# Performance work log

Measured on AMD Instinct MI355X. Metric: run time of the kernel, lower is better.

Reference implementation:

```python
import jax, jax.numpy as jnp
import numpy as np

B, L, H = 2, 2048, 1024
NH, HD = 16, 64  # n_heads, head_size


def setup_inputs() -> dict:
    key = jax.random.key(0)
    ks = jax.random.split(key, 12)
    scale = 1.0 / np.sqrt(H)
    inp = {
        "hidden_states": jax.random.normal(ks[0], (B, L, H), dtype=jnp.float32),
        "tau": jax.random.uniform(ks[1], (B, 1), dtype=jnp.float32) + 0.5,
        "delta": jax.random.normal(ks[2], (B, L), dtype=jnp.float32) * 0.1,
        "Wq": jax.random.normal(ks[3], (H, H), dtype=jnp.float32) * scale,
        "bq": jnp.zeros((H,), dtype=jnp.float32),
        "Wk": jax.random.normal(ks[4], (H, H), dtype=jnp.float32) * scale,
        "bk": jnp.zeros((H,), dtype=jnp.float32),
        "Wv": jax.random.normal(ks[5], (H, H), dtype=jnp.float32) * scale,
        "bv": jnp.zeros((H,), dtype=jnp.float32),
        "Wo": jax.random.normal(ks[6], (H, H), dtype=jnp.float32) * scale,
        "bo": jnp.zeros((H,), dtype=jnp.float32),
    }
    return inp


def _split_heads(x):
    # [B, L, H] -> [B, NH, L, HD]
    return x.reshape(B, L, NH, HD).transpose(0, 2, 1, 3)


def reference(hidden_states, tau, delta, Wq, bq, Wk, bk, Wv, bv, Wo, bo):
    q = _split_heads(hidden_states @ Wq.T + bq)
    k = _split_heads(hidden_states @ Wk.T + bk)
    v = _split_heads(hidden_states @ Wv.T + bv)
    tau_b = tau[:, :, None, None]          # [B,1,1,1]
    delta_b = delta[:, None, None, :]      # [B,1,1,L]
    scores = jnp.einsum('bhqd,bhkd->bhqk', q, k) * tau_b + delta_b
    scores = scores / np.sqrt(HD)
    attn = jax.nn.softmax(scores, axis=-1)  # dropout = identity (eval mode)
    ctx = jnp.einsum('bhqk,bhkd->bhqd', attn, v)
    ctx = ctx.transpose(0, 2, 1, 3).reshape(B, L, H)
    return ctx @ Wo.T + bo
```

## Files before the change

kernel.cpp:

```cpp
#include <hip/hip_runtime.h>

#define B_ 2
#define L_ 2048
#define H_ 1024
#define NH_ 16
#define HD_ 64

using short8 = __attribute__((__ext_vector_type__(8))) short;
using f32x4 = __attribute__((__ext_vector_type__(4))) float;
using f32x16 = __attribute__((__ext_vector_type__(16))) float;
typedef unsigned short u16;
typedef unsigned int u32;

__device__ __forceinline__ u16 f2bf(float f) {
  union { float f; unsigned u; } x{f};
  unsigned u = x.u;
  u = u + 0x7FFFu + ((u >> 16) & 1u);
  return (u16)(u >> 16);
}

__device__ __forceinline__ void gld16(const void* g, void* l) {
  __builtin_amdgcn_global_load_lds(
      (const __attribute__((address_space(1))) void*)g,
      (__attribute__((address_space(3))) void*)l, 16, 0, 0);
}

#define MFMA16(a, b, c) __builtin_amdgcn_mfma_f32_16x16x32_bf16((a), (b), (c), 0, 0, 0)
#define MFMA32(a, b, c) __builtin_amdgcn_mfma_f32_32x32x16_bf16((a), (b), (c), 0, 0, 0)

__global__ void cast_all(const float* __restrict__ hs, const float* __restrict__ Wq,
                         const float* __restrict__ Wk, const float* __restrict__ Wv,
                         const float* __restrict__ Wo, const float* __restrict__ delta,
                         u16* __restrict__ dst, float* __restrict__ dsc) {
  const int t = blockIdx.x * 256 + threadIdx.x;
  const int i = t * 4;
  const float* src;
  int off;
  if (i < 4194304) {
    src = hs; off = i;
  } else {
    const int j = i - 4194304;
    const int w = j >> 20;
    off = j & 1048575;
    src = (w == 0) ? Wq : (w == 1) ? Wk : (w == 2) ? Wv : Wo;
  }
  float4 v = *(const float4*)(src + off);
  *(ushort4*)(dst + i) = make_ushort4(f2bf(v.x), f2bf(v.y), f2bf(v.z), f2bf(v.w));
  if (t < 4096) dsc[t] = delta[t] * 0.18033688011112042f;
}

__global__ __launch_bounds__(512) void gemm_qkv192(
    const u16* __restrict__ A, const u16* __restrict__ W,
    const float* __restrict__ bq, const float* __restrict__ bk, const float* __restrict__ bv,
    const float* __restrict__ tau,
    u16* __restrict__ qg, u16* __restrict__ kg, u16* __restrict__ vTg) {
  __shared__ u16 As[2][256 * 64];
  __shared__ u16 Bs[2][192 * 64];
  const int tid = threadIdx.x;
  const int lane = tid & 63;
  const int wid = tid >> 6;
  const int wr = wid >> 2;
  const int wc = wid & 3;
  const int orig = blockIdx.y * 16 + blockIdx.x;
  const int wg = (orig & 7) * 32 + (orig >> 3);
  const int m0 = (wg & 15) * 256;
  const int n0 = (wg >> 4) * 192;

  const int srow = tid >> 3;
  const int sg = tid & 7;

#define STAGEQ(slot, t_)                                                                \
  {                                                                                     \
    const int kt64 = (t_) * 64;                                                         \
    _Pragma("unroll") for (int li = 0; li < 4; li++) {                                  \
      const int row = li * 64 + srow;                                                   \
      const int gsrc = sg ^ (row & 7);                                                  \
      gld16(A + (size_t)(m0 + row) * 1024 + kt64 + gsrc * 8,                            \
            (char*)As[slot] + li * 8192 + wid * 1024 + lane * 16);                      \
    }                                                                                   \
    _Pragma("unroll") for (int li = 0; li < 3; li++) {                                  \
      const int row = li * 64 + srow;                                                   \
      const int gsrc = sg ^ (row & 7);                                                  \
      gld16(W + (size_t)(n0 + row) * 1024 + kt64 + gsrc * 8,                            \
            (char*)Bs[slot] + li * 8192 + wid * 1024 + lane * 16);                      \
    }                                                                                   \
  }

  f32x4 acc[8][3] = {};

  STAGEQ(0, 0);
  STAGEQ(1, 1);

  for (int t = 0; t < 16; t++) {
    if (t >= 1 && t + 1 < 16) STAGEQ((t + 1) & 1, t + 1);
    if (t + 1 < 16) {
      asm volatile("s_waitcnt vmcnt(7)" ::: "memory");
    } else {
      asm volatile("s_waitcnt vmcnt(0)" ::: "memory");
    }
    asm volatile("s_barrier" ::: "memory");
    const u16* Ab = As[t & 1];
    const u16* Bb = Bs[t & 1];
    short8 bf[3];
#pragma unroll
    for (int q = 0; q < 4; q++) {
      const int mh = q & 1, ks = q >> 1;
      const int g0 = ks * 4 + (lane >> 4);
      if (mh == 0) {
#pragma unroll
        for (int ni = 0; ni < 3; ni++) {
          const int r = wc * 48 + ni * 16 + (lane & 15);
          bf[ni] = *(const short8*)((const char*)Bb + r * 128 + ((g0 ^ (r & 7)) << 4));
        }
      }
      short8 af[4];
#pragma unroll
      for (int mi = 0; mi < 4; mi++) {
        const int r = wr * 128 + (mh * 4 + mi) * 16 + (lane & 15);
        af[mi] = *(const short8*)((const char*)Ab + r * 128 + ((g0 ^ (r & 7)) << 4));
      }
      __builtin_amdgcn_s_setprio(1);
#pragma unroll
      for (int mi = 0; mi < 4; mi++)
#pragma unroll
        for (int ni = 0; ni < 3; ni++)
          acc[mh * 4 + mi][ni] = MFMA16(af[mi], bf[ni], acc[mh * 4 + mi][ni]);
      __builtin_amdgcn_s_setprio(0);
      asm volatile("s_barrier" ::: "memory");
    }
  }

  const int b_blk = m0 >> 11;
  const float tauv = tau[b_blk] * 0.18033688011112042f;
#pragma unroll
  for (int ni = 0; ni < 3; ni++) {
    const int nbase = n0 + wc * 48 + ni * 16;
    const int which = nbase >> 10;
    const int n = nbase + (lane & 15);
    const int nn = n & 1023;
    const int h = nn >> 6, d = nn & 63;
    const float* bias = which == 0 ? bq : (which == 1 ? bk : bv);
    const float bb = bias[nn];
    const float scl = which == 0 ? tauv : 1.0f;
#pragma unroll
    for (int mi = 0; mi < 8; mi++) {
      const int mb = m0 + wr * 128 + mi * 16 + ((lane >> 4) << 2);
      const int b = mb >> 11;
      const int lq = mb & 2047;
      if (which == 2) {
        ushort4 pk = make_ushort4(f2bf(acc[mi][ni][0] + bb), f2bf(acc[mi][ni][1] + bb),
                                  f2bf(acc[mi][ni][2] + bb), f2bf(acc[mi][ni][3] + bb));
        *(ushort4*)&vTg[((size_t)(b * NH_ + h) * HD_ + d) * L_ + lq] = pk;
      } else {
        u16* dst = which == 0 ? qg : kg;
#pragma unroll
        for (int r = 0; r < 4; r++)
          dst[((size_t)(b * NH_ + h) * L_ + lq + r) * HD_ + d] = f2bf((acc[mi][ni][r] + bb) * scl);
      }
    }
  }
}

__global__ __launch_bounds__(512) void attn(
    const u16* __restrict__ qg, const u16* __restrict__ kg, const u16* __restrict__ vTg,
    const float* __restrict__ dsc, u16* __restrict__ ctxg) {
  __shared__ u16 lds[3][8192];
  const int tid = threadIdx.x;
  const int lane = tid & 63;
  const int wv = tid >> 6;
  const int lane31 = lane & 31;
  const int hi = lane >> 5;
  const int orig = blockIdx.x;
  const int wgid = (orig & 7) * 32 + (orig >> 3);
  const int bh = wgid >> 3;
  const int qblk = wgid & 7;
  const int b = bh >> 4;
  const int h = bh & 15;
  const int q0 = qblk * 256 + wv * 32;
  const u16* qb = qg + (size_t)bh * L_ * HD_;
  const u16* kb = kg + (size_t)bh * L_ * HD_;
  const u16* vb = vTg + (size_t)bh * HD_ * L_;
  const float* db = dsc + (size_t)b * L_;

  short8 qf[4];
#pragma unroll
  for (int ks = 0; ks < 4; ks++)
    qf[ks] = *(const short8*)&qb[(size_t)(q0 + lane31) * 64 + ks * 16 + hi * 8];

  union { u32 u[4]; short8 s; } onesu;
  const u32 ow = (lane31 == 0) ? 0x3F803F80u : 0u;
  onesu.u[0] = ow; onesu.u[1] = ow; onesu.u[2] = ow; onesu.u[3] = ow;
  const short8 onesf = onesu.s;

  f32x16 acc[2] = {};
  f32x16 accl = {};
  float mrun = -__builtin_inff();

#define STAGE(bp_, j0)                                                                    \
  {                                                                                       \
    u16* bp = (bp_);                                                                      \
    {                                                                                     \
      const int kt = wv >> 2, ks = wv & 3;                                                \
      gld16(kb + (size_t)((j0) + kt * 32 + lane31) * 64 + ks * 16 + hi * 8,               \
            bp + wv * 512 + lane * 8);                                                    \
    }                                                                                     \
    {                                                                                     \
      const int kt = wv >> 2, dt = (wv >> 1) & 1, ks2 = wv & 1;                           \
      gld16(vb + (size_t)(dt * 32 + lane31) * L_ + (j0) + kt * 32 + ks2 * 16 + hi * 8,    \
            bp + (8 + wv) * 512 + lane * 8);                                              \
    }                                                                                     \
  }

#define QK64(bp_, sA_, sB_)                                                               \
  {                                                                                       \
    const u16* bp = (bp_);                                                                \
    __builtin_amdgcn_s_setprio(1);                                                        \
    _Pragma("unroll") for (int ks = 0; ks < 4; ks++) {                                    \
      short8 kf0 = *(const short8*)&bp[(0 * 4 + ks) * 512 + lane * 8];                    \
      short8 kf1 = *(const short8*)&bp[(1 * 4 + ks) * 512 + lane * 8];                    \
      sA_ = MFMA32(kf0, qf[ks], sA_);                                                     \
      sB_ = MFMA32(kf1, qf[ks], sB_);                                                     \
    }                                                                                     \
    __builtin_amdgcn_s_setprio(0);                                                        \
  }

  STAGE(lds[0], 0);
  STAGE(lds[1], 64);
  __syncthreads();

  f32x16 sp0 = {}, sp1 = {};
  QK64(lds[0], sp0, sp1);

  int cur = 0, nxt = 1, fut = 2;
  for (int t = 0; t < 32; t++) {
    const int j0 = t * 64;
    if (t + 2 < 32) STAGE(lds[fut], j0 + 128);
    f32x16 sn0 = {}, sn1 = {};
    if (t + 1 < 32) QK64(lds[nxt], sn0, sn1);

#pragma unroll
    for (int g = 0; g < 4; g++) {
      float4 dl0 = *(const float4*)&db[j0 + g * 8 + hi * 4];
      float4 dl1 = *(const float4*)&db[j0 + 32 + g * 8 + hi * 4];
      sp0[g * 4 + 0] += dl0.x; sp0[g * 4 + 1] += dl0.y;
      sp0[g * 4 + 2] += dl0.z; sp0[g * 4 + 3] += dl0.w;
      sp1[g * 4 + 0] += dl1.x; sp1[g * 4 + 1] += dl1.y;
      sp1[g * 4 + 2] += dl1.z; sp1[g * 4 + 3] += dl1.w;
    }
    float tm[8];
#pragma unroll
    for (int r = 0; r < 8; r++) tm[r] = fmaxf(fmaxf(sp0[r], sp0[8 + r]), fmaxf(sp1[r], sp1[8 + r]));
#pragma unroll
    for (int r = 0; r < 4; r++) tm[r] = fmaxf(tm[r], tm[4 + r]);
    float pmax = fmaxf(fmaxf(tm[0], tm[1]), fmaxf(tm[2], tm[3]));
    pmax = fmaxf(pmax, __shfl_xor(pmax, 32));
    if (!__all(pmax - mrun <= 11.5f)) {
      float mnew = fmaxf(mrun, pmax);
      float al = __builtin_amdgcn_exp2f(mrun - mnew);
      mrun = mnew;
      accl[0] *= al;
#pragma unroll
      for (int dt = 0; dt < 2; dt++)
#pragma unroll
        for (int r = 0; r < 16; r++) acc[dt][r] *= al;
    }
#pragma unroll
    for (int r = 0; r < 16; r++) {
      sp0[r] = __builtin_amdgcn_exp2f(sp0[r] - mrun);
      sp1[r] = __builtin_amdgcn_exp2f(sp1[r] - mrun);
    }
    u32 pk[16];
#pragma unroll
    for (int i = 0; i < 8; i++) {
      asm("v_cvt_pk_bf16_f32 %0, %1, %2" : "=v"(pk[i]) : "v"(sp0[2 * i]), "v"(sp0[2 * i + 1]));
      asm("v_cvt_pk_bf16_f32 %0, %1, %2" : "=v"(pk[8 + i]) : "v"(sp1[2 * i]), "v"(sp1[2 * i + 1]));
    }
#pragma unroll
    for (int kt = 0; kt < 2; kt++) {
      asm volatile("v_permlane32_swap_b32 %0, %1" : "+v"(pk[kt * 8 + 0]), "+v"(pk[kt * 8 + 2]));
      asm volatile("v_permlane32_swap_b32 %0, %1" : "+v"(pk[kt * 8 + 1]), "+v"(pk[kt * 8 + 3]));
      asm volatile("v_permlane32_swap_b32 %0, %1" : "+v"(pk[kt * 8 + 4]), "+v"(pk[kt * 8 + 6]));
      asm volatile("v_permlane32_swap_b32 %0, %1" : "+v"(pk[kt * 8 + 5]), "+v"(pk[kt * 8 + 7]));
    }
    {
      const u16* bp = lds[cur];
      __builtin_amdgcn_s_setprio(1);
#pragma unroll
      for (int kt = 0; kt < 2; kt++)
#pragma unroll
        for (int ks2 = 0; ks2 < 2; ks2++) {
          union U8 { u32 u[4]; short8 s; } pf;
          pf.u[0] = pk[kt * 8 + ks2 * 4 + 0];
          pf.u[1] = pk[kt * 8 + ks2 * 4 + 1];
          pf.u[2] = pk[kt * 8 + ks2 * 4 + 2];
          pf.u[3] = pk[kt * 8 + ks2 * 4 + 3];
#pragma unroll
          for (int dt = 0; dt < 2; dt++) {
            short8 vf = *(const short8*)&bp[(8 + kt * 4 + dt * 2 + ks2) * 512 + lane * 8];
            acc[dt] = MFMA32(vf, pf.s, acc[dt]);
          }
          accl = MFMA32(onesf, pf.s, accl);
        }
      __builtin_amdgcn_s_setprio(0);
    }
    __syncthreads();
    sp0 = sn0; sp1 = sn1;
    const int tmp = cur; cur = nxt; nxt = fut; fut = tmp;
  }

  u16* tw = (u16*)lds + wv * 2048;
  const float l0 = accl[0];
  const float l1 = __shfl_xor(l0, 32);
  const float inv = 1.0f / (hi ? l1 : l0);
#pragma unroll
  for (int dt = 0; dt < 2; dt++)
#pragma unroll
    for (int g = 0; g < 4; g++) {
      ushort4 w4 = make_ushort4(f2bf(acc[dt][g * 4 + 0] * inv), f2bf(acc[dt][g * 4 + 1] * inv),
                                f2bf(acc[dt][g * 4 + 2] * inv), f2bf(acc[dt][g * 4 + 3] * inv));
      const int d0 = dt * 32 + g * 8 + hi * 4;
      const int byte = (lane31 * 128 + d0 * 2) ^ ((lane31 & 15) << 3);
      *(ushort4*)((char*)tw + byte) = w4;
    }
  asm volatile("s_waitcnt lgkmcnt(0)" ::: "memory");
  const size_t obase = ((size_t)b * L_ + q0) * 1024 + h * 64;
#pragma unroll
  for (int i = 0; i < 16; i++) {
    const int qr = 2 * i + hi;
    const int byte = (qr * 128 + lane31 * 4) ^ ((qr & 15) << 3);
    const u32 val = *(const u32*)((const char*)tw + byte);
    *(u32*)&ctxg[obase + (size_t)qr * 1024 + lane31 * 2] = val;
  }
}

__global__ __launch_bounds__(256) void gemm_out128(
    const u16* __restrict__ A, const u16* __restrict__ W,
    const float* __restrict__ bo, float* __restrict__ out) {
  __shared__ u16 As[2][128 * 64];
  __shared__ u16 Bs[2][128 * 64];
  const int tid = threadIdx.x;
  const int lane = tid & 63;
  const int wid = tid >> 6;
  const int wr = wid >> 1;
  const int wc = wid & 1;
  const int orig = blockIdx.y * 8 + blockIdx.x;
  const int wg = (orig & 7) * 32 + (orig >> 3);
  const int m0 = (wg & 31) * 128;
  const int n0 = (wg >> 5) * 128;

  const int srow = tid >> 3;
  const int sg = tid & 7;

#define STAGEO(slot, t_)                                                                \
  {                                                                                     \
    const int kt64 = (t_) * 64;                                                         \
    _Pragma("unroll") for (int li = 0; li < 4; li++) {                                  \
      const int row = li * 32 + srow;                                                   \
      const int gsrc = sg ^ (row & 7);                                                  \
      gld16(A + (size_t)(m0 + row) * 1024 + kt64 + gsrc * 8,                            \
            (char*)As[slot] + li * 4096 + wid * 1024 + lane * 16);                      \
      gld16(W + (size_t)(n0 + row) * 1024 + kt64 + gsrc * 8,                            \
            (char*)Bs[slot] + li * 4096 + wid * 1024 + lane * 16);                      \
    }                                                                                   \
  }

  f32x4 acc[4][4] = {};

  STAGEO(0, 0);
  STAGEO(1, 1);

  for (int t = 0; t < 16; t++) {
    if (t >= 1 && t + 1 < 16) STAGEO((t + 1) & 1, t + 1);
    if (t + 1 < 16) {
      asm volatile("s_waitcnt vmcnt(8)" ::: "memory");
    } else {
      asm volatile("s_waitcnt vmcnt(0)" ::: "memory");
    }
    asm volatile("s_barrier" ::: "memory");
    const u16* Ab = As[t & 1];
    const u16* Bb = Bs[t & 1];
    short8 bf[4];
#pragma unroll
    for (int q = 0; q < 4; q++) {
      const int mh = q & 1, ks = q >> 1;
      const int g0 = ks * 4 + (lane >> 4);
      if (mh == 0) {
#pragma unroll
        for (int ni = 0; ni < 4; ni++) {
          const int r = wc * 64 + ni * 16 + (lane & 15);
          bf[ni] = *(const short8*)((const char*)Bb + r * 128 + ((g0 ^ (r & 7)) << 4));
        }
      }
      short8 af[2];
#pragma unroll
      for (int mi = 0; mi < 2; mi++) {
        const int r = wr * 64 + (mh * 2 + mi) * 16 + (lane & 15);
        af[mi] = *(const short8*)((const char*)Ab + r * 128 + ((g0 ^ (r & 7)) << 4));
      }
      __builtin_amdgcn_s_setprio(1);
#pragma unroll
      for (int mi = 0; mi < 2; mi++)
#pragma unroll
        for (int ni = 0; ni < 4; ni++)
          acc[mh * 2 + mi][ni] = MFMA16(af[mi], bf[ni], acc[mh * 2 + mi][ni]);
      __builtin_amdgcn_s_setprio(0);
      asm volatile("s_barrier" ::: "memory");
    }
  }

#pragma unroll
  for (int ni = 0; ni < 4; ni++) {
    const int n = n0 + wc * 64 + ni * 16 + (lane & 15);
    const float bb = bo[n];
#pragma unroll
    for (int mi = 0; mi < 4; mi++) {
      const int mb = m0 + wr * 64 + mi * 16 + ((lane >> 4) << 2);
#pragma unroll
      for (int r = 0; r < 4; r++)
        out[(size_t)(mb + r) * 1024 + n] = acc[mi][ni][r] + bb;
    }
  }
}

extern "C" void kernel_launch(void* const* d_in, const int* in_sizes, int n_in,
                              void* d_out, int out_size, void* d_ws, size_t ws_size,
                              hipStream_t stream) {
  const float* hs = (const float*)d_in[0];
  const float* tau = (const float*)d_in[1];
  const float* delta = (const float*)d_in[2];
  const float* Wq = (const float*)d_in[3];
  const float* bq = (const float*)d_in[4];
  const float* Wk = (const float*)d_in[5];
  const float* bk = (const float*)d_in[6];
  const float* Wv = (const float*)d_in[7];
  const float* bv = (const float*)d_in[8];
  const float* Wo = (const float*)d_in[9];
  const float* bo = (const float*)d_in[10];
  float* out = (float*)d_out;

  u16* ws = (u16*)d_ws;
  u16* hsb  = ws;
  u16* wqkv = ws + 4194304;
  u16* wob  = ws + 7340032;
  u16* qg   = ws + 8388608;
  u16* kg   = ws + 12582912;
  u16* vTg  = ws + 16777216;
  u16* ctxg = ws + 20971520;
  float* dsc = (float*)(ws + 25165824);

  cast_all<<<8192, 256, 0, stream>>>(hs, Wq, Wk, Wv, Wo, delta, ws, dsc);

  gemm_qkv192<<<dim3(16, 16), 512, 0, stream>>>(hsb, wqkv, bq, bk, bv, tau, qg, kg, vTg);
  attn<<<256, 512, 0, stream>>>(qg, kg, vTg, dsc, ctxg);
  gemm_out128<<<dim3(8, 32), 256, 0, stream>>>(ctxg, wob, bo, out);
}
```

Before: 139.2 us.

## Fold delta bias into QK MFMA via rank-1 product and split PV by half

The per-key delta bias is now stored as bf16 and added to the scores through an extra rank-1 MFMA, with a one-hot ones vector as the second operand, before the QK^T MFMAs. This replaces the per-iteration float4 global loads and VALU adds. The max reduction is reordered to match, and the exp/convert/PV-MFMA sequence is split into two halves so exponentials of the second half can overlap the first half's MFMAs. In exchange, delta is rounded to bf16 precision, which slightly changes numerics, and each QK tile costs two extra MFMAs.

```diff
diff --git a/kernel.cpp b/kernel.cpp
--- a/kernel.cpp
+++ b/kernel.cpp
@@ -31,7 +31,7 @@
 __global__ void cast_all(const float* __restrict__ hs, const float* __restrict__ Wq,
                          const float* __restrict__ Wk, const float* __restrict__ Wv,
                          const float* __restrict__ Wo, const float* __restrict__ delta,
-                         u16* __restrict__ dst, float* __restrict__ dsc) {
+                         u16* __restrict__ dst, u16* __restrict__ dscb) {
   const int t = blockIdx.x * 256 + threadIdx.x;
   const int i = t * 4;
   const float* src;
@@ -46,7 +46,7 @@
   }
   float4 v = *(const float4*)(src + off);
   *(ushort4*)(dst + i) = make_ushort4(f2bf(v.x), f2bf(v.y), f2bf(v.z), f2bf(v.w));
-  if (t < 4096) dsc[t] = delta[t] * 0.18033688011112042f;
+  if (t < 4096) dscb[t] = f2bf(delta[t] * 0.18033688011112042f);
 }
 
 __global__ __launch_bounds__(512) void gemm_qkv192(
@@ -163,7 +163,7 @@
 
 __global__ __launch_bounds__(512) void attn(
     const u16* __restrict__ qg, const u16* __restrict__ kg, const u16* __restrict__ vTg,
-    const float* __restrict__ dsc, u16* __restrict__ ctxg) {
+    const u16* __restrict__ dscb, u16* __restrict__ ctxg) {
   __shared__ u16 lds[3][8192];
   const int tid = threadIdx.x;
   const int lane = tid & 63;
@@ -180,17 +180,22 @@
   const u16* qb = qg + (size_t)bh * L_ * HD_;
   const u16* kb = kg + (size_t)bh * L_ * HD_;
   const u16* vb = vTg + (size_t)bh * HD_ * L_;
-  const float* db = dsc + (size_t)b * L_;
+  const u16* dbb = dscb + (size_t)b * L_;
 
   short8 qf[4];
 #pragma unroll
   for (int ks = 0; ks < 4; ks++)
     qf[ks] = *(const short8*)&qb[(size_t)(q0 + lane31) * 64 + ks * 16 + hi * 8];
 
-  union { u32 u[4]; short8 s; } onesu;
+  union U8 { u32 u[4]; short8 s; };
+  U8 onesu;
   const u32 ow = (lane31 == 0) ? 0x3F803F80u : 0u;
   onesu.u[0] = ow; onesu.u[1] = ow; onesu.u[2] = ow; onesu.u[3] = ow;
   const short8 onesf = onesu.s;
+  U8 onesbu;
+  onesbu.u[0] = (hi == 0) ? 0x00003F80u : 0u;
+  onesbu.u[1] = 0; onesbu.u[2] = 0; onesbu.u[3] = 0;
+  const short8 onesB = onesbu.s;
 
   f32x16 acc[2] = {};
   f32x16 accl = {};
@@ -211,10 +216,17 @@
     }                                                                                     \
   }
 
-#define QK64(bp_, sA_, sB_)                                                               \
+#define QK64(bp_, j_, sA_, sB_)                                                           \
   {                                                                                       \
     const u16* bp = (bp_);                                                                \
+    U8 df0, df1;                                                                          \
+    df0.u[0] = (hi == 0) ? (u32)dbb[(j_) + lane31] : 0u;                                  \
+    df0.u[1] = 0; df0.u[2] = 0; df0.u[3] = 0;                                             \
+    df1.u[0] = (hi == 0) ? (u32)dbb[(j_) + 32 + lane31] : 0u;                             \
+    df1.u[1] = 0; df1.u[2] = 0; df1.u[3] = 0;                                             \
     __builtin_amdgcn_s_setprio(1);                                                        \
+    sA_ = MFMA32(df0.s, onesB, sA_);                                                      \
+    sB_ = MFMA32(df1.s, onesB, sB_);                                                      \
     _Pragma("unroll") for (int ks = 0; ks < 4; ks++) {                                    \
       short8 kf0 = *(const short8*)&bp[(0 * 4 + ks) * 512 + lane * 8];                    \
       short8 kf1 = *(const short8*)&bp[(1 * 4 + ks) * 512 + lane * 8];                    \
@@ -229,29 +241,22 @@
   __syncthreads();
 
   f32x16 sp0 = {}, sp1 = {};
-  QK64(lds[0], sp0, sp1);
+  QK64(lds[0], 0, sp0, sp1);
 
   int cur = 0, nxt = 1, fut = 2;
   for (int t = 0; t < 32; t++) {
     const int j0 = t * 64;
     if (t + 2 < 32) STAGE(lds[fut], j0 + 128);
     f32x16 sn0 = {}, sn1 = {};
-    if (t + 1 < 32) QK64(lds[nxt], sn0, sn1);
-
-#pragma unroll
-    for (int g = 0; g < 4; g++) {
-      float4 dl0 = *(const float4*)&db[j0 + g * 8 + hi * 4];
-      float4 dl1 = *(const float4*)&db[j0 + 32 + g * 8 + hi * 4];
-      sp0[g * 4 + 0] += dl0.x; sp0[g * 4 + 1] += dl0.y;
-      sp0[g * 4 + 2] += dl0.z; sp0[g * 4 + 3] += dl0.w;
-      sp1[g * 4 + 0] += dl1.x; sp1[g * 4 + 1] += dl1.y;
-      sp1[g * 4 + 2] += dl1.z; sp1[g * 4 + 3] += dl1.w;
-    }
-    float tm[8];
-#pragma unroll
-    for (int r = 0; r < 8; r++) tm[r] = fmaxf(fmaxf(sp0[r], sp0[8 + r]), fmaxf(sp1[r], sp1[8 + r]));
-#pragma unroll
-    for (int r = 0; r < 4; r++) tm[r] = fmaxf(tm[r], tm[4 + r]);
+    if (t + 1 < 32) QK64(lds[nxt], j0 + 64, sn0, sn1);
+
+    float tm[4];
+#pragma unroll
+    for (int r = 0; r < 4; r++) {
+      float a0 = fmaxf(fmaxf(sp0[r], sp0[4 + r]), fmaxf(sp0[8 + r], sp0[12 + r]));
+      float a1 = fmaxf(fmaxf(sp1[r], sp1[4 + r]), fmaxf(sp1[8 + r], sp1[12 + r]));
+      tm[r] = fmaxf(a0, a1);
+    }
     float pmax = fmaxf(fmaxf(tm[0], tm[1]), fmaxf(tm[2], tm[3]));
     pmax = fmaxf(pmax, __shfl_xor(pmax, 32));
     if (!__all(pmax - mrun <= 11.5f)) {
@@ -264,45 +269,56 @@
 #pragma unroll
         for (int r = 0; r < 16; r++) acc[dt][r] *= al;
     }
-#pragma unroll
-    for (int r = 0; r < 16; r++) {
-      sp0[r] = __builtin_amdgcn_exp2f(sp0[r] - mrun);
-      sp1[r] = __builtin_amdgcn_exp2f(sp1[r] - mrun);
-    }
-    u32 pk[16];
-#pragma unroll
-    for (int i = 0; i < 8; i++) {
-      asm("v_cvt_pk_bf16_f32 %0, %1, %2" : "=v"(pk[i]) : "v"(sp0[2 * i]), "v"(sp0[2 * i + 1]));
-      asm("v_cvt_pk_bf16_f32 %0, %1, %2" : "=v"(pk[8 + i]) : "v"(sp1[2 * i]), "v"(sp1[2 * i + 1]));
-    }
-#pragma unroll
-    for (int kt = 0; kt < 2; kt++) {
-      asm volatile("v_permlane32_swap_b32 %0, %1" : "+v"(pk[kt * 8 + 0]), "+v"(pk[kt * 8 + 2]));
-      asm volatile("v_permlane32_swap_b32 %0, %1" : "+v"(pk[kt * 8 + 1]), "+v"(pk[kt * 8 + 3]));
-      asm volatile("v_permlane32_swap_b32 %0, %1" : "+v"(pk[kt * 8 + 4]), "+v"(pk[kt * 8 + 6]));
-      asm volatile("v_permlane32_swap_b32 %0, %1" : "+v"(pk[kt * 8 + 5]), "+v"(pk[kt * 8 + 7]));
-    }
-    {
-      const u16* bp = lds[cur];
-      __builtin_amdgcn_s_setprio(1);
-#pragma unroll
-      for (int kt = 0; kt < 2; kt++)
-#pragma unroll
-        for (int ks2 = 0; ks2 < 2; ks2++) {
-          union U8 { u32 u[4]; short8 s; } pf;
-          pf.u[0] = pk[kt * 8 + ks2 * 4 + 0];
-          pf.u[1] = pk[kt * 8 + ks2 * 4 + 1];
-          pf.u[2] = pk[kt * 8 + ks2 * 4 + 2];
-          pf.u[3] = pk[kt * 8 + ks2 * 4 + 3];
-#pragma unroll
-          for (int dt = 0; dt < 2; dt++) {
-            short8 vf = *(const short8*)&bp[(8 + kt * 4 + dt * 2 + ks2) * 512 + lane * 8];
-            acc[dt] = MFMA32(vf, pf.s, acc[dt]);
-          }
-          accl = MFMA32(onesf, pf.s, accl);
-        }
-      __builtin_amdgcn_s_setprio(0);
-    }
+
+    const u16* bp = lds[cur];
+#pragma unroll
+    for (int r = 0; r < 16; r++) sp0[r] = __builtin_amdgcn_exp2f(sp0[r] - mrun);
+    u32 pk0[8];
+#pragma unroll
+    for (int i = 0; i < 8; i++)
+      asm("v_cvt_pk_bf16_f32 %0, %1, %2" : "=v"(pk0[i]) : "v"(sp0[2 * i]), "v"(sp0[2 * i + 1]));
+    asm volatile("v_permlane32_swap_b32 %0, %1" : "+v"(pk0[0]), "+v"(pk0[2]));
+    asm volatile("v_permlane32_swap_b32 %0, %1" : "+v"(pk0[1]), "+v"(pk0[3]));
+    asm volatile("v_permlane32_swap_b32 %0, %1" : "+v"(pk0[4]), "+v"(pk0[6]));
+    asm volatile("v_permlane32_swap_b32 %0, %1" : "+v"(pk0[5]), "+v"(pk0[7]));
+    __builtin_amdgcn_s_setprio(1);
+#pragma unroll
+    for (int ks2 = 0; ks2 < 2; ks2++) {
+      U8 pf;
+      pf.u[0] = pk0[ks2 * 4 + 0]; pf.u[1] = pk0[ks2 * 4 + 1];
+      pf.u[2] = pk0[ks2 * 4 + 2]; pf.u[3] = pk0[ks2 * 4 + 3];
+#pragma unroll
+      for (int dt = 0; dt < 2; dt++) {
+        short8 vf = *(const short8*)&bp[(8 + 0 * 4 + dt * 2 + ks2) * 512 + lane * 8];
+        acc[dt] = MFMA32(vf, pf.s, acc[dt]);
+      }
+      accl = MFMA32(onesf, pf.s, accl);
+    }
+    __builtin_amdgcn_s_setprio(0);
+#pragma unroll
+    for (int r = 0; r < 16; r++) sp1[r] = __builtin_amdgcn_exp2f(sp1[r] - mrun);
+    u32 pk1[8];
+#pragma unroll
+    for (int i = 0; i < 8; i++)
+      asm("v_cvt_pk_bf16_f32 %0, %1, %2" : "=v"(pk1[i]) : "v"(sp1[2 * i]), "v"(sp1[2 * i + 1]));
+    asm volatile("v_permlane32_swap_b32 %0, %1" : "+v"(pk1[0]), "+v"(pk1[2]));
+    asm volatile("v_permlane32_swap_b32 %0, %1" : "+v"(pk1[1]), "+v"(pk1[3]));
+    asm volatile("v_permlane32_swap_b32 %0, %1" : "+v"(pk1[4]), "+v"(pk1[6]));
+    asm volatile("v_permlane32_swap_b32 %0, %1" : "+v"(pk1[5]), "+v"(pk1[7]));
+    __builtin_amdgcn_s_setprio(1);
+#pragma unroll
+    for (int ks2 = 0; ks2 < 2; ks2++) {
+      U8 pf;
+      pf.u[0] = pk1[ks2 * 4 + 0]; pf.u[1] = pk1[ks2 * 4 + 1];
+      pf.u[2] = pk1[ks2 * 4 + 2]; pf.u[3] = pk1[ks2 * 4 + 3];
+#pragma unroll
+      for (int dt = 0; dt < 2; dt++) {
+        short8 vf = *(const short8*)&bp[(8 + 1 * 4 + dt * 2 + ks2) * 512 + lane * 8];
+        acc[dt] = MFMA32(vf, pf.s, acc[dt]);
+      }
+      accl = MFMA32(onesf, pf.s, accl);
+    }
+    __builtin_amdgcn_s_setprio(0);
     __syncthreads();
     sp0 = sn0; sp1 = sn1;
     const int tmp = cur; cur = nxt; nxt = fut; fut = tmp;
@@ -446,11 +462,11 @@
   u16* kg   = ws + 12582912;
   u16* vTg  = ws + 16777216;
   u16* ctxg = ws + 20971520;
-  float* dsc = (float*)(ws + 25165824);
-
-  cast_all<<<8192, 256, 0, stream>>>(hs, Wq, Wk, Wv, Wo, delta, ws, dsc);
+  u16* dscb = ws + 25165824;
+
+  cast_all<<<8192, 256, 0, stream>>>(hs, Wq, Wk, Wv, Wo, delta, ws, dscb);
 
   gemm_qkv192<<<dim3(16, 16), 512, 0, stream>>>(hsb, wqkv, bq, bk, bv, tau, qg, kg, vTg);
-  attn<<<256, 512, 0, stream>>>(qg, kg, vTg, dsc, ctxg);
+  attn<<<256, 512, 0, stream>>>(qg, kg, vTg, dscb, ctxg);
   gemm_out128<<<dim3(8, 32), 256, 0, stream>>>(ctxg, wob, bo, out);
 }
```

Result: faster. 132.9 us, median of 2 (-4.5%).
